# Performance work log

Measured on AMD Instinct MI355X. Metric: run time of the kernel, lower is better.

Reference implementation:

```python
import jax, jax.numpy as jnp
import numpy as np

B, C, H, W, N_REF = 4, 256, 128, 128, 4


def setup_inputs() -> dict:
    key = jax.random.key(0)
    ks = jax.random.split(key, 9)
    s = 1.0 / np.sqrt(C)
    x = jax.random.normal(ks[0], (B, C, H, W), jnp.float32)
    Wq = jax.random.normal(ks[1], (C, C), jnp.float32) * s
    bq = jax.random.normal(ks[2], (C,), jnp.float32) * 0.01
    Wk = jax.random.normal(ks[3], (C, C), jnp.float32) * s
    bk = jax.random.normal(ks[4], (C,), jnp.float32) * 0.01
    Wv = jax.random.normal(ks[5], (C, C), jnp.float32) * s
    bv = jax.random.normal(ks[6], (C,), jnp.float32) * 0.01
    Wo = jax.random.normal(ks[7], (2 * N_REF, C), jnp.float32) * s
    bo = jax.random.normal(ks[8], (2 * N_REF,), jnp.float32) * 0.01
    return {"x": x, "Wq": Wq, "bq": bq, "Wk": Wk, "bk": bk,
            "Wv": Wv, "bv": bv, "Wo": Wo, "bo": bo}


def _proj(Wt, bt, x):
    # 1x1 conv == per-pixel channel matmul
    return jnp.einsum('oc,bchw->bohw', Wt, x) + bt[None, :, None, None]


def reference(x, Wq, bq, Wk, bk, Wv, bv, Wo, bo):
    b, c, h, w = x.shape
    n = Wo.shape[0] // 2
    hw = h * w

    Q = _proj(Wq, bq, x)
    K = _proj(Wk, bk, x)
    V = _proj(Wv, bv, x)

    offsets = _proj(Wo, bo, Q).reshape(b, n, 2, h, w)

    grid_w = jnp.arange(w, dtype=jnp.float32)[None, None, None, :]
    grid_h = jnp.arange(h, dtype=jnp.float32)[None, None, :, None]
    # clamp then truncate toward zero (matches torch .clamp().long() for >=0 values)
    ref_w = jnp.clip(grid_w + offsets[:, :, 0], 0, w - 1)
    ref_h = jnp.clip(grid_h + offsets[:, :, 1], 0, h - 1)
    idx = (jax.lax.stop_gradient(ref_h).astype(jnp.int32) * w
           + jax.lax.stop_gradient(ref_w).astype(jnp.int32)).reshape(b, n * hw)

    K_flat = K.reshape(b, c, hw)
    V_flat = V.reshape(b, c, hw)
    Kg = jnp.take_along_axis(K_flat, idx[:, None, :], axis=2).reshape(b, c, n, hw)
    Vg = jnp.take_along_axis(V_flat, idx[:, None, :], axis=2).reshape(b, c, n, hw)

    Q_flat = Q.reshape(b, c, hw)
    # NOTE: original module applies no softmax/scale — raw dot-product weights
    attn = jnp.einsum('bch,bcnh->bnh', Q_flat, Kg)
    out = jnp.einsum('bnh,bcnh->bch', attn, Vg)
    return out.reshape(b, c, h, w)
```

## Files before the change

### kernel.cpp

```cpp
#include <hip/hip_runtime.h>

#define HW   16384
#define CH   256
#define WD   128
#define NPTS 4

typedef _Float16 half8 __attribute__((ext_vector_type(8)));
typedef _Float16 half4 __attribute__((ext_vector_type(4)));
typedef float    f32x4 __attribute__((ext_vector_type(4)));

#define WS_XT    0ull
#define WS_WQK   33554432ull
#define WS_WV    33685504ull
#define WS_WOQ   33816576ull
#define WS_BOF   33824768ull
#define WS_CVEC  33824832ull
#define WS_DVEC  33825856ull
#define WS_SC    33826880ull
#define WS_SVEC  33826944ull
#define WS_IDX   34089088ull

__global__ void k_wprep(const float* __restrict__ Wq, const float* __restrict__ bq,
                        const float* __restrict__ Wk, const float* __restrict__ bk,
                        const float* __restrict__ Wv, const float* __restrict__ bv,
                        const float* __restrict__ Wo, const float* __restrict__ bo,
                        _Float16* __restrict__ wqk16, float* __restrict__ cvec,
                        _Float16* __restrict__ wv16, float* __restrict__ woq,
                        float* __restrict__ bof, float* __restrict__ dvec,
                        float* __restrict__ scst) {
    int bid = blockIdx.x, t = threadIdx.x;
    if (bid < 256) {
        int i = bid;
        float s = 0.f;
        for (int o = 0; o < 256; o++) s += Wk[o * 256 + i] * Wq[o * 256 + t];
        wqk16[i * 256 + t] = (_Float16)s;
        if (t == 0) {
            float cs = 0.f;
            for (int o = 0; o < 256; o++) cs += Wk[o * 256 + i] * bq[o];
            cvec[i] = cs;
        }
    } else if (bid < 512) {
        int r = bid - 256;
        wv16[r * 256 + t] = (_Float16)Wv[r * 256 + t];
    } else if (bid < 520) {
        int j = bid - 512;
        float s = 0.f;
        for (int o = 0; o < 256; o++) s += Wo[j * 256 + o] * Wq[o * 256 + t];
        woq[t * 8 + j] = s;
        if (t == 0) {
            float tt = bo[j];
            for (int o = 0; o < 256; o++) tt += Wo[j * 256 + o] * bq[o];
            bof[j] = tt;
        }
    } else {
        float s = 0.f;
        for (int o = 0; o < 256; o++) s += bk[o] * Wq[o * 256 + t];
        dvec[t] = s;
        if (t == 0) {
            float sc = 0.f;
            for (int o = 0; o < 256; o++) sc += bq[o] * bk[o];
            scst[0] = sc;
        }
    }
}

__launch_bounds__(256)
__global__ void k_prep(const float* __restrict__ x, const float* __restrict__ woq,
                       const float* __restrict__ bof, const float* __restrict__ dvec,
                       const float* __restrict__ scst,
                       _Float16* __restrict__ xt, int* __restrict__ idxb,
                       float* __restrict__ svec) {
    __shared__ float    wl[256 * 8];
    __shared__ float    dl[256];
    __shared__ float    bl8[8];
    __shared__ _Float16 tile[64][280];
    __shared__ float    red[4][64][8];
    __shared__ float    reds[4][64];

    int t = threadIdx.x;
    for (int i = t; i < 256 * 8; i += 256) wl[i] = woq[i];
    dl[t] = dvec[t];
    if (t < 8) bl8[t] = bof[t];
    __syncthreads();

    int b = blockIdx.y;
    int p0 = blockIdx.x * 64;
    int pl = t & 63, cg = t >> 6;
    const float* xb = x + (size_t)b * CH * HW + p0 + pl;

    float acc[8];
    #pragma unroll
    for (int j = 0; j < 8; j++) acc[j] = 0.f;
    float accs = 0.f;

    for (int i0 = 0; i0 < 64; i0 += 8) {
        half8 hv;
        #pragma unroll
        for (int i = 0; i < 8; i++) {
            int c = cg * 64 + i0 + i;
            float xv = xb[(size_t)c * HW];
            hv[i] = (_Float16)xv;
            accs += dl[c] * xv;
            #pragma unroll
            for (int j = 0; j < 8; j++) acc[j] += wl[c * 8 + j] * xv;
        }
        *(half8*)(&tile[pl][cg * 64 + i0]) = hv;
    }
    #pragma unroll
    for (int j = 0; j < 8; j++) red[cg][pl][j] = acc[j];
    reds[cg][pl] = accs;
    __syncthreads();

    {
        int n = cg, p = p0 + pl;
        float sw_ = bl8[2 * n]     + red[0][pl][2 * n]     + red[1][pl][2 * n]
                                   + red[2][pl][2 * n]     + red[3][pl][2 * n];
        float sh_ = bl8[2 * n + 1] + red[0][pl][2 * n + 1] + red[1][pl][2 * n + 1]
                                   + red[2][pl][2 * n + 1] + red[3][pl][2 * n + 1];
        int h = p >> 7, w = p & 127;
        float rw = fminf(fmaxf((float)w + sw_, 0.f), 127.f);
        float rh = fminf(fmaxf((float)h + sh_, 0.f), 127.f);
        idxb[(b * NPTS + n) * HW + p] = ((int)rh) * WD + (int)rw;
        if (cg == 0)
            svec[b * HW + p] = reds[0][pl] + reds[1][pl] + reds[2][pl] + reds[3][pl] + scst[0];
    }

    {
        int row = t >> 2;
        size_t gbase = ((size_t)(b * HW + p0 + row)) * 256;
        #pragma unroll
        for (int s = 0; s < 8; s++) {
            int seg = (t & 3) + s * 4;
            *(uint4*)(xt + gbase + seg * 8) = *(const uint4*)(&tile[row][seg * 8]);
        }
    }
}

__launch_bounds__(512)
__global__ void k_fused(const _Float16* __restrict__ xt, const _Float16* __restrict__ wqk16,
                        const _Float16* __restrict__ wv16, const float* __restrict__ cvec,
                        const float* __restrict__ bv, const int* __restrict__ idxb,
                        const float* __restrict__ svec, float* __restrict__ out) {
    __shared__ _Float16 AQW[64 * 256];
    __shared__ _Float16 Bs[2][256 * 32];
    __shared__ float    asf[64];

    int tid = threadIdx.x;
    int b = blockIdx.y;
    int bx = blockIdx.x;
    int logical = (bx & 7) * 32 + (bx >> 3);
    int p0 = logical * 64;
    size_t mrow0 = (size_t)b * HW + p0;

    int lane = tid & 63, wid = tid >> 6;
    int wr = wid >> 2, wc = wid & 3;
    int g = lane >> 4, r = lane & 15;

    {
        int row = tid >> 3;
        int c0 = tid & 7;
        const uint4* src = (const uint4*)(xt + (mrow0 + row) * 256);
        #pragma unroll
        for (int s = 0; s < 4; s++) {
            int c8 = c0 + s * 8;
            uint4 v = src[c8];
            *(uint4*)(&AQW[(row << 8) + 8 * (c8 ^ (row & 7))]) = v;
        }
    }

    int brow = tid >> 1, bseg = tid & 1;
    int bslot0 = (bseg * 2)     ^ ((brow >> 1) & 3);
    int bslot1 = (bseg * 2 + 1) ^ ((brow >> 1) & 3);
    uint4 br0, br1;

    {
        const _Float16* p = wqk16 + (size_t)brow * 256 + bseg * 16;
        br0 = *(const uint4*)(p);
        br1 = *(const uint4*)(p + 8);
        *(uint4*)(&Bs[0][brow * 32 + bslot0 * 8]) = br0;
        *(uint4*)(&Bs[0][brow * 32 + bslot1 * 8]) = br1;
        p += 32;
        br0 = *(const uint4*)(p);
        br1 = *(const uint4*)(p + 8);
    }

    int seg = tid & 15, pslot = tid >> 4;
    int jj0[NPTS], jj1[NPTS];
    #pragma unroll
    for (int n = 0; n < NPTS; n++) {
        jj0[n] = idxb[(b * NPTS + n) * HW + p0 + pslot];
        jj1[n] = idxb[(b * NPTS + n) * HW + p0 + 32 + pslot];
    }
    float sv0 = svec[mrow0 + pslot];
    float sv1 = svec[mrow0 + 32 + pslot];
    __syncthreads();

    f32x4 acc[2][4] = {};
    #pragma unroll
    for (int kt = 0; kt < 8; kt++) {
        if (kt < 7) {
            _Float16* B = &Bs[(kt + 1) & 1][0];
            *(uint4*)(&B[brow * 32 + bslot0 * 8]) = br0;
            *(uint4*)(&B[brow * 32 + bslot1 * 8]) = br1;
        }
        if (kt < 6) {
            const _Float16* p = wqk16 + (size_t)brow * 256 + (kt + 2) * 32 + bseg * 16;
            br0 = *(const uint4*)(p);
            br1 = *(const uint4*)(p + 8);
        }
        half8 af[2], bf[4];
        #pragma unroll
        for (int mb = 0; mb < 2; mb++) {
            int row = wr * 32 + mb * 16 + r;
            af[mb] = *(const half8*)(&AQW[(row << 8) + ((kt * 32 + g * 8) ^ ((row & 7) << 3))]);
        }
        #pragma unroll
        for (int nb = 0; nb < 4; nb++) {
            int row = wc * 64 + nb * 16 + r;
            bf[nb] = *(const half8*)(&Bs[kt & 1][row * 32 + ((g ^ ((row >> 1) & 3)) << 3)]);
        }
        #pragma unroll
        for (int mb = 0; mb < 2; mb++)
            #pragma unroll
            for (int nb = 0; nb < 4; nb++)
                acc[mb][nb] = __builtin_amdgcn_mfma_f32_16x16x32_f16(bf[nb], af[mb], acc[mb][nb], 0, 0, 0);
        __syncthreads();
    }

    #pragma unroll
    for (int mb = 0; mb < 2; mb++) {
        int row = wr * 32 + mb * 16 + r;
        #pragma unroll
        for (int nb = 0; nb < 4; nb++) {
            int ncol = wc * 64 + nb * 16 + g * 4;
            f32x4 cv = *(const f32x4*)(cvec + ncol);
            half4 h;
            #pragma unroll
            for (int i = 0; i < 4; i++) h[i] = (_Float16)(acc[mb][nb][i] + cv[i]);
            *(half4*)(&AQW[(row << 8) + (ncol ^ ((row & 7) << 3))]) = h;
        }
    }
    __syncthreads();

    {
        const _Float16* p = wv16 + (size_t)brow * 256 + bseg * 16;
        br0 = *(const uint4*)(p);
        br1 = *(const uint4*)(p + 8);
        *(uint4*)(&Bs[0][brow * 32 + bslot0 * 8]) = br0;
        *(uint4*)(&Bs[0][brow * 32 + bslot1 * 8]) = br1;
        p += 32;
        br0 = *(const uint4*)(p);
        br1 = *(const uint4*)(p + 8);
    }

    {
        half8 xva[NPTS], xvb[NPTS], xvc[NPTS], xvd[NPTS];
        #pragma unroll
        for (int n = 0; n < NPTS; n++) {
            const _Float16* xr = xt + ((size_t)b * HW + jj0[n]) * 256;
            xva[n] = *(const half8*)(xr + seg * 8);
            xvb[n] = *(const half8*)(xr + 128 + seg * 8);
        }
        #pragma unroll
        for (int n = 0; n < NPTS; n++) {
            const _Float16* xr = xt + ((size_t)b * HW + jj1[n]) * 256;
            xvc[n] = *(const half8*)(xr + seg * 8);
            xvd[n] = *(const half8*)(xr + 128 + seg * 8);
        }

        {
            int pl = pslot;
            int qa0 = (pl << 8) + ((seg * 8)       ^ ((pl & 7) << 3));
            int qa1 = (pl << 8) + ((128 + seg * 8) ^ ((pl & 7) << 3));
            half8 q0 = *(const half8*)(&AQW[qa0]);
            half8 q1 = *(const half8*)(&AQW[qa1]);
            float o0[8], o1[8];
            #pragma unroll
            for (int e = 0; e < 8; e++) { o0[e] = 0.f; o1[e] = 0.f; }
            float asl = 0.f;
            #pragma unroll
            for (int n = 0; n < NPTS; n++) {
                float d = 0.f;
                #pragma unroll
                for (int e = 0; e < 8; e++) d += (float)q0[e] * (float)xva[n][e];
                #pragma unroll
                for (int e = 0; e < 8; e++) d += (float)q1[e] * (float)xvb[n][e];
                d += __shfl_xor(d, 1);
                d += __shfl_xor(d, 2);
                d += __shfl_xor(d, 4);
                d += __shfl_xor(d, 8);
                float a = d + sv0;
                asl += a;
                #pragma unroll
                for (int e = 0; e < 8; e++) o0[e] += a * (float)xva[n][e];
                #pragma unroll
                for (int e = 0; e < 8; e++) o1[e] += a * (float)xvb[n][e];
            }
            half8 h0, h1;
            #pragma unroll
            for (int e = 0; e < 8; e++) { h0[e] = (_Float16)o0[e]; h1[e] = (_Float16)o1[e]; }
            *(half8*)(&AQW[qa0]) = h0;
            *(half8*)(&AQW[qa1]) = h1;
            if (seg == 0) asf[pl] = asl;
        }

        {
            int pl = 32 + pslot;
            int qa0 = (pl << 8) + ((seg * 8)       ^ ((pl & 7) << 3));
            int qa1 = (pl << 8) + ((128 + seg * 8) ^ ((pl & 7) << 3));
            half8 q0 = *(const half8*)(&AQW[qa0]);
            half8 q1 = *(const half8*)(&AQW[qa1]);
            float o0[8], o1[8];
            #pragma unroll
            for (int e = 0; e < 8; e++) { o0[e] = 0.f; o1[e] = 0.f; }
            float asl = 0.f;
            #pragma unroll
            for (int n = 0; n < NPTS; n++) {
                float d = 0.f;
                #pragma unroll
                for (int e = 0; e < 8; e++) d += (float)q0[e] * (float)xvc[n][e];
                #pragma unroll
                for (int e = 0; e < 8; e++) d += (float)q1[e] * (float)xvd[n][e];
                d += __shfl_xor(d, 1);
                d += __shfl_xor(d, 2);
                d += __shfl_xor(d, 4);
                d += __shfl_xor(d, 8);
                float a = d + sv1;
                asl += a;
                #pragma unroll
                for (int e = 0; e < 8; e++) o0[e] += a * (float)xvc[n][e];
                #pragma unroll
                for (int e = 0; e < 8; e++) o1[e] += a * (float)xvd[n][e];
            }
            half8 h0, h1;
            #pragma unroll
            for (int e = 0; e < 8; e++) { h0[e] = (_Float16)o0[e]; h1[e] = (_Float16)o1[e]; }
            *(half8*)(&AQW[qa0]) = h0;
            *(half8*)(&AQW[qa1]) = h1;
            if (seg == 0) asf[pl] = asl;
        }
    }
    __syncthreads();

    f32x4 acc2[2][4] = {};
    #pragma unroll
    for (int kt = 0; kt < 8; kt++) {
        if (kt < 7) {
            _Float16* B = &Bs[(kt + 1) & 1][0];
            *(uint4*)(&B[brow * 32 + bslot0 * 8]) = br0;
            *(uint4*)(&B[brow * 32 + bslot1 * 8]) = br1;
        }
        if (kt < 6) {
            const _Float16* p = wv16 + (size_t)brow * 256 + (kt + 2) * 32 + bseg * 16;
            br0 = *(const uint4*)(p);
            br1 = *(const uint4*)(p + 8);
        }
        half8 af[2], bf[4];
        #pragma unroll
        for (int mb = 0; mb < 2; mb++) {
            int row = wr * 32 + mb * 16 + r;
            af[mb] = *(const half8*)(&AQW[(row << 8) + ((kt * 32 + g * 8) ^ ((row & 7) << 3))]);
        }
        #pragma unroll
        for (int nb = 0; nb < 4; nb++) {
            int row = wc * 64 + nb * 16 + r;
            bf[nb] = *(const half8*)(&Bs[kt & 1][row * 32 + ((g ^ ((row >> 1) & 3)) << 3)]);
        }
        #pragma unroll
        for (int mb = 0; mb < 2; mb++)
            #pragma unroll
            for (int nb = 0; nb < 4; nb++)
                acc2[mb][nb] = __builtin_amdgcn_mfma_f32_16x16x32_f16(bf[nb], af[mb], acc2[mb][nb], 0, 0, 0);
        __syncthreads();
    }

    #pragma unroll
    for (int mb = 0; mb < 2; mb++) {
        int mrow = wr * 32 + mb * 16 + r;
        float am = asf[mrow];
        float* obase = out + (size_t)b * CH * HW + p0 + mrow;
        #pragma unroll
        for (int nb = 0; nb < 4; nb++) {
            int cb = wc * 64 + nb * 16 + g * 4;
            f32x4 bb = *(const f32x4*)(bv + cb);
            #pragma unroll
            for (int i = 0; i < 4; i++)
                obase[(size_t)(cb + i) * HW] = acc2[mb][nb][i] + am * bb[i];
        }
    }
}

extern "C" void kernel_launch(void* const* d_in, const int* in_sizes, int n_in,
                              void* d_out, int out_size, void* d_ws, size_t ws_size,
                              hipStream_t stream) {
    const float* x  = (const float*)d_in[0];
    const float* Wq = (const float*)d_in[1];
    const float* bq = (const float*)d_in[2];
    const float* Wk = (const float*)d_in[3];
    const float* bk = (const float*)d_in[4];
    const float* Wv = (const float*)d_in[5];
    const float* bv = (const float*)d_in[6];
    const float* Wo = (const float*)d_in[7];
    const float* bo = (const float*)d_in[8];
    (void)in_sizes; (void)n_in; (void)out_size; (void)ws_size;

    char* ws = (char*)d_ws;
    _Float16* xt    = (_Float16*)(ws + WS_XT);
    _Float16* wqk16 = (_Float16*)(ws + WS_WQK);
    _Float16* wv16  = (_Float16*)(ws + WS_WV);
    float*    woq   = (float*)(ws + WS_WOQ);
    float*    bof   = (float*)(ws + WS_BOF);
    float*    cvec  = (float*)(ws + WS_CVEC);
    float*    dvec  = (float*)(ws + WS_DVEC);
    float*    scst  = (float*)(ws + WS_SC);
    float*    svec  = (float*)(ws + WS_SVEC);
    int*      idxb  = (int*)(ws + WS_IDX);

    k_wprep<<<521, 256, 0, stream>>>(Wq, bq, Wk, bk, Wv, bv, Wo, bo,
                                     wqk16, cvec, wv16, woq, bof, dvec, scst);
    k_prep<<<dim3(256, 4), 256, 0, stream>>>(x, woq, bof, dvec, scst, xt, idxb, svec);
    k_fused<<<dim3(256, 4), 512, 0, stream>>>(xt, wqk16, wv16, cvec, bv, idxb, svec,
                                              (float*)d_out);
}
```

Baseline: 88.73 us.

## Load weight fragments directly from global into registers, dropping LDS staging

```diff
diff --git a/kernel.cpp b/kernel.cpp
--- a/kernel.cpp
+++ b/kernel.cpp
@@ -142,7 +142,6 @@
                         const float* __restrict__ bv, const int* __restrict__ idxb,
                         const float* __restrict__ svec, float* __restrict__ out) {
     __shared__ _Float16 AQW[64 * 256];
-    __shared__ _Float16 Bs[2][256 * 32];
     __shared__ float    asf[64];
 
     int tid = threadIdx.x;
@@ -168,22 +167,6 @@
         }
     }
 
-    int brow = tid >> 1, bseg = tid & 1;
-    int bslot0 = (bseg * 2)     ^ ((brow >> 1) & 3);
-    int bslot1 = (bseg * 2 + 1) ^ ((brow >> 1) & 3);
-    uint4 br0, br1;
-
-    {
-        const _Float16* p = wqk16 + (size_t)brow * 256 + bseg * 16;
-        br0 = *(const uint4*)(p);
-        br1 = *(const uint4*)(p + 8);
-        *(uint4*)(&Bs[0][brow * 32 + bslot0 * 8]) = br0;
-        *(uint4*)(&Bs[0][brow * 32 + bslot1 * 8]) = br1;
-        p += 32;
-        br0 = *(const uint4*)(p);
-        br1 = *(const uint4*)(p + 8);
-    }
-
     int seg = tid & 15, pslot = tid >> 4;
     int jj0[NPTS], jj1[NPTS];
     #pragma unroll
@@ -193,39 +176,39 @@
     }
     float sv0 = svec[mrow0 + pslot];
     float sv1 = svec[mrow0 + 32 + pslot];
+
+    const _Float16* Bq = wqk16 + (size_t)(wc * 64 + r) * 256 + g * 8;
+    const _Float16* Bv = wv16  + (size_t)(wc * 64 + r) * 256 + g * 8;
+
+    half8 bfc[4], bfn[4];
+    #pragma unroll
+    for (int nb = 0; nb < 4; nb++) bfc[nb] = *(const half8*)(Bq + nb * 16 * 256);
+
     __syncthreads();
 
     f32x4 acc[2][4] = {};
-    #pragma unroll
+    #pragma unroll 1
     for (int kt = 0; kt < 8; kt++) {
         if (kt < 7) {
-            _Float16* B = &Bs[(kt + 1) & 1][0];
-            *(uint4*)(&B[brow * 32 + bslot0 * 8]) = br0;
-            *(uint4*)(&B[brow * 32 + bslot1 * 8]) = br1;
-        }
-        if (kt < 6) {
-            const _Float16* p = wqk16 + (size_t)brow * 256 + (kt + 2) * 32 + bseg * 16;
-            br0 = *(const uint4*)(p);
-            br1 = *(const uint4*)(p + 8);
-        }
-        half8 af[2], bf[4];
+            #pragma unroll
+            for (int nb = 0; nb < 4; nb++)
+                bfn[nb] = *(const half8*)(Bq + nb * 16 * 256 + (kt + 1) * 32);
+        }
+        half8 af[2];
         #pragma unroll
         for (int mb = 0; mb < 2; mb++) {
             int row = wr * 32 + mb * 16 + r;
             af[mb] = *(const half8*)(&AQW[(row << 8) + ((kt * 32 + g * 8) ^ ((row & 7) << 3))]);
         }
         #pragma unroll
-        for (int nb = 0; nb < 4; nb++) {
-            int row = wc * 64 + nb * 16 + r;
-            bf[nb] = *(const half8*)(&Bs[kt & 1][row * 32 + ((g ^ ((row >> 1) & 3)) << 3)]);
-        }
-        #pragma unroll
         for (int mb = 0; mb < 2; mb++)
             #pragma unroll
             for (int nb = 0; nb < 4; nb++)
-                acc[mb][nb] = __builtin_amdgcn_mfma_f32_16x16x32_f16(bf[nb], af[mb], acc[mb][nb], 0, 0, 0);
-        __syncthreads();
-    }
+                acc[mb][nb] = __builtin_amdgcn_mfma_f32_16x16x32_f16(bfc[nb], af[mb], acc[mb][nb], 0, 0, 0);
+        #pragma unroll
+        for (int nb = 0; nb < 4; nb++) bfc[nb] = bfn[nb];
+    }
+    __syncthreads();
 
     #pragma unroll
     for (int mb = 0; mb < 2; mb++) {
@@ -241,17 +224,6 @@
         }
     }
     __syncthreads();
-
-    {
-        const _Float16* p = wv16 + (size_t)brow * 256 + bseg * 16;
-        br0 = *(const uint4*)(p);
-        br1 = *(const uint4*)(p + 8);
-        *(uint4*)(&Bs[0][brow * 32 + bslot0 * 8]) = br0;
-        *(uint4*)(&Bs[0][brow * 32 + bslot1 * 8]) = br1;
-        p += 32;
-        br0 = *(const uint4*)(p);
-        br1 = *(const uint4*)(p + 8);
-    }
 
     {
         half8 xva[NPTS], xvb[NPTS], xvc[NPTS], xvd[NPTS];
@@ -340,38 +312,32 @@
             if (seg == 0) asf[pl] = asl;
         }
     }
+
+    #pragma unroll
+    for (int nb = 0; nb < 4; nb++) bfc[nb] = *(const half8*)(Bv + nb * 16 * 256);
     __syncthreads();
 
     f32x4 acc2[2][4] = {};
-    #pragma unroll
+    #pragma unroll 1
     for (int kt = 0; kt < 8; kt++) {
         if (kt < 7) {
-            _Float16* B = &Bs[(kt + 1) & 1][0];
-            *(uint4*)(&B[brow * 32 + bslot0 * 8]) = br0;
-            *(uint4*)(&B[brow * 32 + bslot1 * 8]) = br1;
-        }
-        if (kt < 6) {
-            const _Float16* p = wv16 + (size_t)brow * 256 + (kt + 2) * 32 + bseg * 16;
-            br0 = *(const uint4*)(p);
-            br1 = *(const uint4*)(p + 8);
-        }
-        half8 af[2], bf[4];
+            #pragma unroll
+            for (int nb = 0; nb < 4; nb++)
+                bfn[nb] = *(const half8*)(Bv + nb * 16 * 256 + (kt + 1) * 32);
+        }
+        half8 af[2];
         #pragma unroll
         for (int mb = 0; mb < 2; mb++) {
             int row = wr * 32 + mb * 16 + r;
             af[mb] = *(const half8*)(&AQW[(row << 8) + ((kt * 32 + g * 8) ^ ((row & 7) << 3))]);
         }
         #pragma unroll
-        for (int nb = 0; nb < 4; nb++) {
-            int row = wc * 64 + nb * 16 + r;
-            bf[nb] = *(const half8*)(&Bs[kt & 1][row * 32 + ((g ^ ((row >> 1) & 3)) << 3)]);
-        }
-        #pragma unroll
         for (int mb = 0; mb < 2; mb++)
             #pragma unroll
             for (int nb = 0; nb < 4; nb++)
-                acc2[mb][nb] = __builtin_amdgcn_mfma_f32_16x16x32_f16(bf[nb], af[mb], acc2[mb][nb], 0, 0, 0);
-        __syncthreads();
+                acc2[mb][nb] = __builtin_amdgcn_mfma_f32_16x16x32_f16(bfc[nb], af[mb], acc2[mb][nb], 0, 0, 0);
+        #pragma unroll
+        for (int nb = 0; nb < 4; nb++) bfc[nb] = bfn[nb];
     }
 
     #pragma unroll
```

Result: slower. 121.9 us (+37.4%).

## Split weight-prep kernel with 4-way reduction split and raise MFMA wave priority

Applied to the files above, without the earlier changes.

```diff
diff --git a/kernel.cpp b/kernel.cpp
--- a/kernel.cpp
+++ b/kernel.cpp
@@ -20,30 +20,38 @@
 #define WS_SVEC  33826944ull
 #define WS_IDX   34089088ull
 
-__global__ void k_wprep(const float* __restrict__ Wq, const float* __restrict__ bq,
-                        const float* __restrict__ Wk, const float* __restrict__ bk,
-                        const float* __restrict__ Wv, const float* __restrict__ bv,
+__global__ void k_wA(const float* __restrict__ Wq, const float* __restrict__ bq,
+                     const float* __restrict__ Wk,
+                     _Float16* __restrict__ wqk16, float* __restrict__ cvec) {
+    __shared__ float red[4][256];
+    int i = blockIdx.x;
+    int c = threadIdx.x & 255, oq = threadIdx.x >> 8;
+    float s = 0.f;
+    #pragma unroll 4
+    for (int o = oq * 64; o < oq * 64 + 64; o++)
+        s += Wk[o * 256 + i] * Wq[o * 256 + c];
+    red[oq][c] = s;
+    __syncthreads();
+    if (oq == 0)
+        wqk16[i * 256 + c] = (_Float16)(red[0][c] + red[1][c] + red[2][c] + red[3][c]);
+    if (threadIdx.x == 0) {
+        float cs = 0.f;
+        for (int o = 0; o < 256; o++) cs += Wk[o * 256 + i] * bq[o];
+        cvec[i] = cs;
+    }
+}
+
+__global__ void k_wrest(const float* __restrict__ Wq, const float* __restrict__ bq,
+                        const float* __restrict__ bk, const float* __restrict__ Wv,
                         const float* __restrict__ Wo, const float* __restrict__ bo,
-                        _Float16* __restrict__ wqk16, float* __restrict__ cvec,
                         _Float16* __restrict__ wv16, float* __restrict__ woq,
                         float* __restrict__ bof, float* __restrict__ dvec,
                         float* __restrict__ scst) {
     int bid = blockIdx.x, t = threadIdx.x;
     if (bid < 256) {
-        int i = bid;
-        float s = 0.f;
-        for (int o = 0; o < 256; o++) s += Wk[o * 256 + i] * Wq[o * 256 + t];
-        wqk16[i * 256 + t] = (_Float16)s;
-        if (t == 0) {
-            float cs = 0.f;
-            for (int o = 0; o < 256; o++) cs += Wk[o * 256 + i] * bq[o];
-            cvec[i] = cs;
-        }
-    } else if (bid < 512) {
-        int r = bid - 256;
-        wv16[r * 256 + t] = (_Float16)Wv[r * 256 + t];
-    } else if (bid < 520) {
-        int j = bid - 512;
+        wv16[bid * 256 + t] = (_Float16)Wv[bid * 256 + t];
+    } else if (bid < 264) {
+        int j = bid - 256;
         float s = 0.f;
         for (int o = 0; o < 256; o++) s += Wo[j * 256 + o] * Wq[o * 256 + t];
         woq[t * 8 + j] = s;
@@ -219,11 +227,13 @@
             int row = wc * 64 + nb * 16 + r;
             bf[nb] = *(const half8*)(&Bs[kt & 1][row * 32 + ((g ^ ((row >> 1) & 3)) << 3)]);
         }
+        __builtin_amdgcn_s_setprio(1);
         #pragma unroll
         for (int mb = 0; mb < 2; mb++)
             #pragma unroll
             for (int nb = 0; nb < 4; nb++)
                 acc[mb][nb] = __builtin_amdgcn_mfma_f32_16x16x32_f16(bf[nb], af[mb], acc[mb][nb], 0, 0, 0);
+        __builtin_amdgcn_s_setprio(0);
         __syncthreads();
     }
 
@@ -366,11 +376,13 @@
             int row = wc * 64 + nb * 16 + r;
             bf[nb] = *(const half8*)(&Bs[kt & 1][row * 32 + ((g ^ ((row >> 1) & 3)) << 3)]);
         }
+        __builtin_amdgcn_s_setprio(1);
         #pragma unroll
         for (int mb = 0; mb < 2; mb++)
             #pragma unroll
             for (int nb = 0; nb < 4; nb++)
                 acc2[mb][nb] = __builtin_amdgcn_mfma_f32_16x16x32_f16(bf[nb], af[mb], acc2[mb][nb], 0, 0, 0);
+        __builtin_amdgcn_s_setprio(0);
         __syncthreads();
     }
 
@@ -416,8 +428,8 @@
     float*    svec  = (float*)(ws + WS_SVEC);
     int*      idxb  = (int*)(ws + WS_IDX);
 
-    k_wprep<<<521, 256, 0, stream>>>(Wq, bq, Wk, bk, Wv, bv, Wo, bo,
-                                     wqk16, cvec, wv16, woq, bof, dvec, scst);
+    k_wrest<<<265, 256, 0, stream>>>(Wq, bq, bk, Wv, Wo, bo, wv16, woq, bof, dvec, scst);
+    k_wA<<<256, 1024, 0, stream>>>(Wq, bq, Wk, wqk16, cvec);
     k_prep<<<dim3(256, 4), 256, 0, stream>>>(x, woq, bof, dvec, scst, xt, idxb, svec);
     k_fused<<<dim3(256, 4), 512, 0, stream>>>(xt, wqk16, wv16, cvec, bv, idxb, svec,
                                               (float*)d_out);
```

New measurement: 106.0 us. +19.5%, slower.
